# Kernel optimization log

Measured on AMD Instinct MI355X. Metric: run time of the kernel, lower is better.

## Reference

```python
import jax, jax.numpy as jnp
import numpy as np

DIM = 768
HEADS = 16
HEAD_DIM = DIM // HEADS  # 48


def setup_inputs() -> dict:
    key = jax.random.key(0)
    ks = jax.random.split(key, 9)
    s = 1.0 / np.sqrt(DIM)
    inp = {
        "x": jax.random.normal(ks[0], (4, 2048, DIM), dtype=jnp.float32),
        "Wq": jax.random.uniform(ks[1], (DIM, DIM), jnp.float32, -s, s),
        "bq": jax.random.uniform(ks[2], (DIM,), jnp.float32, -s, s),
        "Wk": jax.random.uniform(ks[3], (DIM, DIM), jnp.float32, -s, s),
        "bk": jax.random.uniform(ks[4], (DIM,), jnp.float32, -s, s),
        "Wv": jax.random.uniform(ks[5], (DIM, DIM), jnp.float32, -s, s),
        "bv": jax.random.uniform(ks[6], (DIM,), jnp.float32, -s, s),
        "Wo": jax.random.uniform(ks[7], (DIM, DIM), jnp.float32, -s, s),
        "bo": jax.random.uniform(ks[8], (DIM,), jnp.float32, -s, s),
    }
    return inp


def reference(x, Wq, bq, Wk, bk, Wv, bv, Wo, bo):
    B, S, _ = x.shape
    # torch nn.Linear: y = x @ W.T + b
    q = x @ Wq.T + bq
    k = x @ Wk.T + bk
    v = x @ Wv.T + bv
    # split heads: (B, H, S, Dh)
    q = q.reshape(B, S, HEADS, HEAD_DIM).transpose(0, 2, 1, 3)
    k = k.reshape(B, S, HEADS, HEAD_DIM).transpose(0, 2, 1, 3)
    v = v.reshape(B, S, HEADS, HEAD_DIM).transpose(0, 2, 1, 3)
    score = jnp.einsum("bhqd,bhkd->bhqk", q, k) / jnp.sqrt(jnp.float32(HEAD_DIM))
    attn = jax.nn.softmax(score, axis=-1)
    out = jnp.einsum("bhqk,bhkd->bhqd", attn, v)
    out = out.transpose(0, 2, 1, 3).reshape(B, S, DIM)
    return out @ Wo.T + bo
```

## Files before the change

kernel.cpp:

```cpp
#include <hip/hip_runtime.h>

#define DIM 768
#define SEQ 2048
#define NB 4
#define NH 16
#define DH 48
#define DP 64
#define BHN (NB*NH)
#define MTOK (NB*SEQ)

typedef __attribute__((ext_vector_type(8))) short bf16x8;
typedef __attribute__((ext_vector_type(4))) float f32x4;
typedef __attribute__((ext_vector_type(4))) unsigned int u32x4;

__device__ __forceinline__ unsigned short f32_to_bf16(float f) {
    union { float f; unsigned int u; } v; v.f = f;
    unsigned int r = v.u + 0x7fff + ((v.u >> 16) & 1);
    return (unsigned short)(r >> 16);
}

#if __has_builtin(__builtin_amdgcn_exp2f)
#define EXP2F(x) __builtin_amdgcn_exp2f(x)
#else
#define EXP2F(x) exp2f(x)
#endif

#define GL_LDS16(g, l) __builtin_amdgcn_global_load_lds( \
    (const __attribute__((address_space(1))) void*)(g),  \
    (__attribute__((address_space(3))) void*)(l), 16, 0, 0)

__global__ void cvt_f32_bf16(const float* __restrict__ src, unsigned short* __restrict__ dst, int n) {
    int i = (blockIdx.x * blockDim.x + threadIdx.x) * 4;
    if (i + 3 < n) {
        const float4 v = *(const float4*)(src + i);
        ushort4 o;
        o.x = f32_to_bf16(v.x); o.y = f32_to_bf16(v.y);
        o.z = f32_to_bf16(v.z); o.w = f32_to_bf16(v.w);
        *(ushort4*)(dst + i) = o;
    }
}

__global__ void cvt4_f32_bf16(const float* __restrict__ a, const float* __restrict__ b,
                              const float* __restrict__ c, const float* __restrict__ d,
                              unsigned short* __restrict__ dst, int n_each) {
    const float* srcs[4] = {a, b, c, d};
    const float* src = srcs[blockIdx.y];
    unsigned short* out = dst + blockIdx.y * n_each;
    int i = (blockIdx.x * blockDim.x + threadIdx.x) * 4;
    if (i + 3 < n_each) {
        const float4 v = *(const float4*)(src + i);
        ushort4 o;
        o.x = f32_to_bf16(v.x); o.y = f32_to_bf16(v.y);
        o.z = f32_to_bf16(v.z); o.w = f32_to_bf16(v.w);
        *(ushort4*)(out + i) = o;
    }
}

#define BK 32

__global__ __launch_bounds__(256) void qkv_gemm(
    const unsigned short* __restrict__ xb,
    const unsigned short* __restrict__ wb,
    const float* __restrict__ bq, const float* __restrict__ bk, const float* __restrict__ bv,
    unsigned short* __restrict__ Qb, unsigned short* __restrict__ Kb, unsigned short* __restrict__ Vt)
{
    const int z = blockIdx.z;
    const unsigned short* W = wb + z * (DIM * DIM);
    const float* bias = (z == 0) ? bq : (z == 1) ? bk : bv;
    const int row0 = blockIdx.x * 128;
    const int col0 = blockIdx.y * 128;

    __shared__ __align__(16) short As[128 * BK];
    __shared__ __align__(16) short Bs[128 * BK];

    const int tid = threadIdx.x;
    const int lane = tid & 63;
    const int w = tid >> 6;
    const int wy = w >> 1, wx = w & 1;
    const int l15 = lane & 15, quad = lane >> 4;
    const int lr = lane >> 2;
    const int lco = (lane & 3) * 8;

    f32x4 acc[4][4];
    for (int mi = 0; mi < 4; ++mi) for (int ni = 0; ni < 4; ++ni)
        for (int r = 0; r < 4; ++r) acc[mi][ni][r] = 0.f;

    for (int kt = 0; kt < DIM / BK; ++kt) {
        #pragma unroll
        for (int j = 0; j < 2; ++j) {
            const int c = w * 2 + j;
            GL_LDS16(&xb[(row0 + c * 16 + lr) * DIM + kt * BK + lco], &As[c * 512]);
            GL_LDS16(&W [(col0 + c * 16 + lr) * DIM + kt * BK + lco], &Bs[c * 512]);
        }
        __syncthreads();
        bf16x8 af[4], bfr[4];
        #pragma unroll
        for (int mi = 0; mi < 4; ++mi)
            af[mi] = *(const bf16x8*)&As[(wy * 64 + mi * 16 + l15) * BK + quad * 8];
        #pragma unroll
        for (int ni = 0; ni < 4; ++ni)
            bfr[ni] = *(const bf16x8*)&Bs[(wx * 64 + ni * 16 + l15) * BK + quad * 8];
        #pragma unroll
        for (int mi = 0; mi < 4; ++mi)
            #pragma unroll
            for (int ni = 0; ni < 4; ++ni)
                acc[mi][ni] = __builtin_amdgcn_mfma_f32_16x16x32_bf16(af[mi], bfr[ni], acc[mi][ni], 0, 0, 0);
        __syncthreads();
    }

    const float qscale = 0.14433756729740643f * 1.4426950408889634f;

    if (z == 2) {
        #pragma unroll
        for (int mi = 0; mi < 4; ++mi) {
            #pragma unroll
            for (int ni = 0; ni < 4; ++ni) {
                int col = col0 + wx * 64 + ni * 16 + l15;
                int h = col / DH, d = col - h * DH;
                int row = row0 + wy * 64 + mi * 16 + quad * 4;
                int b = row >> 11, s = row & 2047;
                float bi = bias[col];
                union { ushort4 v; unsigned short e[4]; } pk;
                #pragma unroll
                for (int r = 0; r < 4; ++r)
                    pk.e[r] = f32_to_bf16(acc[mi][ni][r] + bi);
                *(ushort4*)&Vt[((b * NH + h) * DP + d) * SEQ + s] = pk.v;
            }
        }
    } else {
        #pragma unroll
        for (int mi = 0; mi < 4; ++mi) {
            #pragma unroll
            for (int ni = 0; ni < 4; ++ni) {
                #pragma unroll
                for (int r = 0; r < 4; ++r) {
                    int row = row0 + wy * 64 + mi * 16 + quad * 4 + r;
                    int col = col0 + wx * 64 + ni * 16 + l15;
                    float v = acc[mi][ni][r] + bias[col];
                    int b = row >> 11, s = row & 2047;
                    int h = col / DH, d = col - h * DH;
                    int bh = b * NH + h;
                    if (z == 0) Qb[(bh * SEQ + s) * DP + d] = f32_to_bf16(v * qscale);
                    else        Kb[(bh * SEQ + s) * DP + d] = f32_to_bf16(v);
                }
            }
        }
    }
}

__global__ __launch_bounds__(256) void out_gemm(
    const unsigned short* __restrict__ ab,
    const unsigned short* __restrict__ Wo,
    const float* __restrict__ bo,
    float* __restrict__ out)
{
    const int row0 = blockIdx.x * 128;
    const int col0 = blockIdx.y * 128;

    __shared__ __align__(16) short As[128 * BK];
    __shared__ __align__(16) short Bs[128 * BK];

    const int tid = threadIdx.x;
    const int lane = tid & 63;
    const int w = tid >> 6;
    const int wy = w >> 1, wx = w & 1;
    const int l15 = lane & 15, quad = lane >> 4;
    const int lr = lane >> 2;
    const int lco = (lane & 3) * 8;

    f32x4 acc[4][4];
    for (int mi = 0; mi < 4; ++mi) for (int ni = 0; ni < 4; ++ni)
        for (int r = 0; r < 4; ++r) acc[mi][ni][r] = 0.f;

    for (int kt = 0; kt < DIM / BK; ++kt) {
        #pragma unroll
        for (int j = 0; j < 2; ++j) {
            const int c = w * 2 + j;
            GL_LDS16(&ab[(row0 + c * 16 + lr) * DIM + kt * BK + lco], &As[c * 512]);
            GL_LDS16(&Wo[(col0 + c * 16 + lr) * DIM + kt * BK + lco], &Bs[c * 512]);
        }
        __syncthreads();
        bf16x8 af[4], bfr[4];
        #pragma unroll
        for (int mi = 0; mi < 4; ++mi)
            af[mi] = *(const bf16x8*)&As[(wy * 64 + mi * 16 + l15) * BK + quad * 8];
        #pragma unroll
        for (int ni = 0; ni < 4; ++ni)
            bfr[ni] = *(const bf16x8*)&Bs[(wx * 64 + ni * 16 + l15) * BK + quad * 8];
        #pragma unroll
        for (int mi = 0; mi < 4; ++mi)
            #pragma unroll
            for (int ni = 0; ni < 4; ++ni)
                acc[mi][ni] = __builtin_amdgcn_mfma_f32_16x16x32_bf16(af[mi], bfr[ni], acc[mi][ni], 0, 0, 0);
        __syncthreads();
    }

    #pragma unroll
    for (int mi = 0; mi < 4; ++mi)
        #pragma unroll
        for (int ni = 0; ni < 4; ++ni)
            #pragma unroll
            for (int r = 0; r < 4; ++r) {
                int row = row0 + wy * 64 + mi * 16 + quad * 4 + r;
                int col = col0 + wx * 64 + ni * 16 + l15;
                out[row * DIM + col] = acc[mi][ni][r] + bo[col];
            }
}

__device__ __forceinline__ int keyperm(int a) {
    return (a & 32) + ((a & 12) << 1) + ((a & 16) >> 2) + (a & 3);
}

__global__ __launch_bounds__(256, 2) void attn_kernel(
    const unsigned short* __restrict__ Qb,
    const unsigned short* __restrict__ Kb,
    const unsigned short* __restrict__ Vt,
    unsigned short* __restrict__ Ob)
{
    const int bh = blockIdx.x;
    const int tile = blockIdx.y;
    const int tid = threadIdx.x;
    const int w = tid >> 6;
    const int lane = tid & 63;
    const int l15 = lane & 15, quad = lane >> 4;

    const unsigned short* Qh = Qb + bh * SEQ * DP;
    const unsigned short* Kh = Kb + bh * SEQ * DP;
    const unsigned short* Vh = Vt + bh * DP * SEQ;
    const int q0 = tile * 256 + w * 64;

    __shared__ __align__(16) short Ks[64 * 64];
    __shared__ __align__(16) short Vs[48 * 64];

    bf16x8 aq[4][2];
    #pragma unroll
    for (int m = 0; m < 4; ++m)
        #pragma unroll
        for (int ks = 0; ks < 2; ++ks)
            aq[m][ks] = *(const bf16x8*)&Qh[(q0 + m * 16 + l15) * DP + ks * 32 + quad * 8];
    if (quad >= 2) {
        const bf16x8 z8 = {0, 0, 0, 0, 0, 0, 0, 0};
        #pragma unroll
        for (int m = 0; m < 4; ++m) aq[m][1] = z8;
    }

    f32x4 o[4][3];
    #pragma unroll
    for (int m = 0; m < 4; ++m) for (int ni = 0; ni < 3; ++ni)
        for (int r = 0; r < 4; ++r) o[m][ni][r] = 0.f;
    float ls[4][2];
    #pragma unroll
    for (int m = 0; m < 4; ++m) { ls[m][0] = 0.f; ls[m][1] = 0.f; }

    const f32x4 FZ = {0.f, 0.f, 0.f, 0.f};

    const int ra = tid >> 2;
    const int pc = tid & 3;
    const int lcA = ((pc ^ (ra & 7)) * 8);
    const int lcB = (((pc + 4) ^ (ra & 7)) * 8);
    const int kaR = keyperm(ra);
    const int ldsA = ra * 64 + pc * 8;
    const int ldsB = ra * 64 + (pc + 4) * 8;
    const bool vld = (tid < 192);

    bf16x8 kr0, kr1, vr0, vr1;
    kr0 = *(const bf16x8*)&Kh[kaR * DP + lcA];
    kr1 = *(const bf16x8*)&Kh[kaR * DP + lcB];
    if (vld) {
        vr0 = *(const bf16x8*)&Vh[ra * SEQ + lcA];
        vr1 = *(const bf16x8*)&Vh[ra * SEQ + lcB];
    }

    for (int kt = 0; kt < SEQ / 64; ++kt) {
        __syncthreads();
        *(bf16x8*)&Ks[ldsA] = kr0;
        *(bf16x8*)&Ks[ldsB] = kr1;
        if (vld) {
            *(bf16x8*)&Vs[ldsA] = vr0;
            *(bf16x8*)&Vs[ldsB] = vr1;
        }
        if (kt + 1 < SEQ / 64) {
            const int k0n = (kt + 1) * 64;
            kr0 = *(const bf16x8*)&Kh[(k0n + kaR) * DP + lcA];
            kr1 = *(const bf16x8*)&Kh[(k0n + kaR) * DP + lcB];
            if (vld) {
                vr0 = *(const bf16x8*)&Vh[ra * SEQ + k0n + lcA];
                vr1 = *(const bf16x8*)&Vh[ra * SEQ + k0n + lcB];
            }
        }
        __syncthreads();

        bf16x8 ak0[4], ak1[4];
        #pragma unroll
        for (int n = 0; n < 4; ++n) {
            ak0[n] = *(const bf16x8*)&Ks[(n * 16 + l15) * 64 + ((quad ^ (l15 & 7)) * 8)];
            ak1[n] = *(const bf16x8*)&Ks[(n * 16 + l15) * 64 + (((4 + quad) ^ (l15 & 7)) * 8)];
        }
        bf16x8 av[2][3];
        #pragma unroll
        for (int ks = 0; ks < 2; ++ks)
            #pragma unroll
            for (int mt = 0; mt < 3; ++mt)
                av[ks][mt] = *(const bf16x8*)&Vs[(mt * 16 + l15) * 64 + (((ks * 4 + quad) ^ (l15 & 7)) * 8)];

        #pragma unroll
        for (int mp = 0; mp < 2; ++mp) {
            const int m0 = 2 * mp, m1 = 2 * mp + 1;
            f32x4 sc[2][4];
            #pragma unroll
            for (int n = 0; n < 4; ++n) {
                sc[0][n] = __builtin_amdgcn_mfma_f32_16x16x32_bf16(ak0[n], aq[m0][0], FZ, 0, 0, 0);
                sc[1][n] = __builtin_amdgcn_mfma_f32_16x16x32_bf16(ak0[n], aq[m1][0], FZ, 0, 0, 0);
            }
            #pragma unroll
            for (int n = 0; n < 4; ++n) {
                sc[0][n] = __builtin_amdgcn_mfma_f32_16x16x32_bf16(ak1[n], aq[m0][1], sc[0][n], 0, 0, 0);
                sc[1][n] = __builtin_amdgcn_mfma_f32_16x16x32_bf16(ak1[n], aq[m1][1], sc[1][n], 0, 0, 0);
            }
            union { u32x4 u; bf16x8 h; } bp[2][2];
            #pragma unroll
            for (int mi = 0; mi < 2; ++mi) {
                #pragma unroll
                for (int ks = 0; ks < 2; ++ks) {
                    #pragma unroll
                    for (int w2 = 0; w2 < 4; ++w2) {
                        const int j0 = 2 * w2, j1 = 2 * w2 + 1;
                        float p0 = EXP2F(sc[mi][2 * ks + (j0 >> 2)][j0 & 3]);
                        float p1 = EXP2F(sc[mi][2 * ks + (j1 >> 2)][j1 & 3]);
                        ls[2 * mp + mi][w2 & 1] += (p0 + p1);
                        bp[mi][ks].u[w2] = __builtin_amdgcn_perm(__float_as_uint(p1), __float_as_uint(p0), 0x07060302u);
                    }
                }
            }
            #pragma unroll
            for (int ks = 0; ks < 2; ++ks)
                #pragma unroll
                for (int mt = 0; mt < 3; ++mt) {
                    o[m0][mt] = __builtin_amdgcn_mfma_f32_16x16x32_bf16(av[ks][mt], bp[0][ks].h, o[m0][mt], 0, 0, 0);
                    o[m1][mt] = __builtin_amdgcn_mfma_f32_16x16x32_bf16(av[ks][mt], bp[1][ks].h, o[m1][mt], 0, 0, 0);
                }
        }
    }

    const int b = bh >> 4, h = bh & 15;
    #pragma unroll
    for (int m = 0; m < 4; ++m) {
        float lsum = ls[m][0] + ls[m][1];
        lsum += __shfl_xor(lsum, 16);
        lsum += __shfl_xor(lsum, 32);
        float inv = 1.f / lsum;
        #pragma unroll
        for (int mt = 0; mt < 3; ++mt)
            #pragma unroll
            for (int r = 0; r < 4; ++r) {
                int token = b * SEQ + q0 + m * 16 + l15;
                int d = mt * 16 + quad * 4 + r;
                Ob[token * DIM + h * DH + d] = f32_to_bf16(o[m][mt][r] * inv);
            }
    }
}

extern "C" void kernel_launch(void* const* d_in, const int* in_sizes, int n_in,
                              void* d_out, int out_size, void* d_ws, size_t ws_size,
                              hipStream_t stream) {
    const float* x  = (const float*)d_in[0];
    const float* Wq = (const float*)d_in[1]; const float* bq = (const float*)d_in[2];
    const float* Wk = (const float*)d_in[3]; const float* bk = (const float*)d_in[4];
    const float* Wv = (const float*)d_in[5]; const float* bv = (const float*)d_in[6];
    const float* Wo = (const float*)d_in[7]; const float* bo = (const float*)d_in[8];

    unsigned char* ws = (unsigned char*)d_ws;
    unsigned short* xb = (unsigned short*)(ws);
    unsigned short* wb = (unsigned short*)(ws + 12582912);
    unsigned short* Qb = (unsigned short*)(ws + 17301504);
    unsigned short* Kb = (unsigned short*)(ws + 34078720);
    unsigned short* Vt = (unsigned short*)(ws + 50855936);
    unsigned short* Ob = (unsigned short*)(ws + 67633152);

    cvt_f32_bf16<<<6144, 256, 0, stream>>>(x, xb, MTOK * DIM);
    cvt4_f32_bf16<<<dim3(576, 4), 256, 0, stream>>>(Wq, Wk, Wv, Wo, wb, DIM * DIM);

    qkv_gemm<<<dim3(MTOK / 128, DIM / 128, 3), 256, 0, stream>>>(xb, wb, bq, bk, bv, Qb, Kb, Vt);
    attn_kernel<<<dim3(BHN, SEQ / 256), 256, 0, stream>>>(Qb, Kb, Vt, Ob);
    out_gemm<<<dim3(MTOK / 128, DIM / 128), 256, 0, stream>>>(Ob, wb + 3 * DIM * DIM, bo, (float*)d_out);
}
```

Before: 218.9 us.

## Halve attention query tile per block, raise occupancy, add MFMA priority hints

The attention kernel now processes 128 queries per block (32 per wave) instead of 256, doubling the grid and raising launch bounds to 4 blocks per CU to increase occupancy and parallelism. MFMA sections are wrapped in s_setprio to favor matrix issue across waves, and output stores are packed into ushort4 vector writes. The trade-off is that each K/V tile loaded into LDS is reused by half as many queries, doubling K/V global and LDS traffic.

```diff
diff --git a/kernel.cpp b/kernel.cpp
--- a/kernel.cpp
+++ b/kernel.cpp
@@ -211,7 +211,7 @@
     return (a & 32) + ((a & 12) << 1) + ((a & 16) >> 2) + (a & 3);
 }
 
-__global__ __launch_bounds__(256, 2) void attn_kernel(
+__global__ __launch_bounds__(256, 4) void attn_kernel(
     const unsigned short* __restrict__ Qb,
     const unsigned short* __restrict__ Kb,
     const unsigned short* __restrict__ Vt,
@@ -227,30 +227,30 @@
     const unsigned short* Qh = Qb + bh * SEQ * DP;
     const unsigned short* Kh = Kb + bh * SEQ * DP;
     const unsigned short* Vh = Vt + bh * DP * SEQ;
-    const int q0 = tile * 256 + w * 64;
+    const int q0 = tile * 128 + w * 32;
 
     __shared__ __align__(16) short Ks[64 * 64];
     __shared__ __align__(16) short Vs[48 * 64];
 
-    bf16x8 aq[4][2];
-    #pragma unroll
-    for (int m = 0; m < 4; ++m)
+    bf16x8 aq[2][2];
+    #pragma unroll
+    for (int m = 0; m < 2; ++m)
         #pragma unroll
         for (int ks = 0; ks < 2; ++ks)
             aq[m][ks] = *(const bf16x8*)&Qh[(q0 + m * 16 + l15) * DP + ks * 32 + quad * 8];
     if (quad >= 2) {
         const bf16x8 z8 = {0, 0, 0, 0, 0, 0, 0, 0};
         #pragma unroll
-        for (int m = 0; m < 4; ++m) aq[m][1] = z8;
-    }
-
-    f32x4 o[4][3];
-    #pragma unroll
-    for (int m = 0; m < 4; ++m) for (int ni = 0; ni < 3; ++ni)
+        for (int m = 0; m < 2; ++m) aq[m][1] = z8;
+    }
+
+    f32x4 o[2][3];
+    #pragma unroll
+    for (int m = 0; m < 2; ++m) for (int ni = 0; ni < 3; ++ni)
         for (int r = 0; r < 4; ++r) o[m][ni][r] = 0.f;
-    float ls[4][2];
-    #pragma unroll
-    for (int m = 0; m < 4; ++m) { ls[m][0] = 0.f; ls[m][1] = 0.f; }
+    float ls[2][2];
+    #pragma unroll
+    for (int m = 0; m < 2; ++m) { ls[m][0] = 0.f; ls[m][1] = 0.f; }
 
     const f32x4 FZ = {0.f, 0.f, 0.f, 0.f};
 
@@ -303,60 +303,61 @@
             for (int mt = 0; mt < 3; ++mt)
                 av[ks][mt] = *(const bf16x8*)&Vs[(mt * 16 + l15) * 64 + (((ks * 4 + quad) ^ (l15 & 7)) * 8)];
 
-        #pragma unroll
-        for (int mp = 0; mp < 2; ++mp) {
-            const int m0 = 2 * mp, m1 = 2 * mp + 1;
-            f32x4 sc[2][4];
-            #pragma unroll
-            for (int n = 0; n < 4; ++n) {
-                sc[0][n] = __builtin_amdgcn_mfma_f32_16x16x32_bf16(ak0[n], aq[m0][0], FZ, 0, 0, 0);
-                sc[1][n] = __builtin_amdgcn_mfma_f32_16x16x32_bf16(ak0[n], aq[m1][0], FZ, 0, 0, 0);
-            }
-            #pragma unroll
-            for (int n = 0; n < 4; ++n) {
-                sc[0][n] = __builtin_amdgcn_mfma_f32_16x16x32_bf16(ak1[n], aq[m0][1], sc[0][n], 0, 0, 0);
-                sc[1][n] = __builtin_amdgcn_mfma_f32_16x16x32_bf16(ak1[n], aq[m1][1], sc[1][n], 0, 0, 0);
-            }
-            union { u32x4 u; bf16x8 h; } bp[2][2];
-            #pragma unroll
-            for (int mi = 0; mi < 2; ++mi) {
+        f32x4 sc[2][4];
+        __builtin_amdgcn_s_setprio(1);
+        #pragma unroll
+        for (int n = 0; n < 4; ++n) {
+            sc[0][n] = __builtin_amdgcn_mfma_f32_16x16x32_bf16(ak0[n], aq[0][0], FZ, 0, 0, 0);
+            sc[1][n] = __builtin_amdgcn_mfma_f32_16x16x32_bf16(ak0[n], aq[1][0], FZ, 0, 0, 0);
+        }
+        #pragma unroll
+        for (int n = 0; n < 4; ++n) {
+            sc[0][n] = __builtin_amdgcn_mfma_f32_16x16x32_bf16(ak1[n], aq[0][1], sc[0][n], 0, 0, 0);
+            sc[1][n] = __builtin_amdgcn_mfma_f32_16x16x32_bf16(ak1[n], aq[1][1], sc[1][n], 0, 0, 0);
+        }
+        __builtin_amdgcn_s_setprio(0);
+        union { u32x4 u; bf16x8 h; } bp[2][2];
+        #pragma unroll
+        for (int mi = 0; mi < 2; ++mi) {
+            #pragma unroll
+            for (int ks = 0; ks < 2; ++ks) {
                 #pragma unroll
-                for (int ks = 0; ks < 2; ++ks) {
-                    #pragma unroll
-                    for (int w2 = 0; w2 < 4; ++w2) {
-                        const int j0 = 2 * w2, j1 = 2 * w2 + 1;
-                        float p0 = EXP2F(sc[mi][2 * ks + (j0 >> 2)][j0 & 3]);
-                        float p1 = EXP2F(sc[mi][2 * ks + (j1 >> 2)][j1 & 3]);
-                        ls[2 * mp + mi][w2 & 1] += (p0 + p1);
-                        bp[mi][ks].u[w2] = __builtin_amdgcn_perm(__float_as_uint(p1), __float_as_uint(p0), 0x07060302u);
-                    }
+                for (int w2 = 0; w2 < 4; ++w2) {
+                    const int j0 = 2 * w2, j1 = 2 * w2 + 1;
+                    float p0 = EXP2F(sc[mi][2 * ks + (j0 >> 2)][j0 & 3]);
+                    float p1 = EXP2F(sc[mi][2 * ks + (j1 >> 2)][j1 & 3]);
+                    ls[mi][w2 & 1] += (p0 + p1);
+                    bp[mi][ks].u[w2] = __builtin_amdgcn_perm(__float_as_uint(p1), __float_as_uint(p0), 0x07060302u);
                 }
             }
-            #pragma unroll
-            for (int ks = 0; ks < 2; ++ks)
-                #pragma unroll
-                for (int mt = 0; mt < 3; ++mt) {
-                    o[m0][mt] = __builtin_amdgcn_mfma_f32_16x16x32_bf16(av[ks][mt], bp[0][ks].h, o[m0][mt], 0, 0, 0);
-                    o[m1][mt] = __builtin_amdgcn_mfma_f32_16x16x32_bf16(av[ks][mt], bp[1][ks].h, o[m1][mt], 0, 0, 0);
-                }
-        }
+        }
+        __builtin_amdgcn_s_setprio(1);
+        #pragma unroll
+        for (int ks = 0; ks < 2; ++ks)
+            #pragma unroll
+            for (int mt = 0; mt < 3; ++mt) {
+                o[0][mt] = __builtin_amdgcn_mfma_f32_16x16x32_bf16(av[ks][mt], bp[0][ks].h, o[0][mt], 0, 0, 0);
+                o[1][mt] = __builtin_amdgcn_mfma_f32_16x16x32_bf16(av[ks][mt], bp[1][ks].h, o[1][mt], 0, 0, 0);
+            }
+        __builtin_amdgcn_s_setprio(0);
     }
 
     const int b = bh >> 4, h = bh & 15;
     #pragma unroll
-    for (int m = 0; m < 4; ++m) {
+    for (int m = 0; m < 2; ++m) {
         float lsum = ls[m][0] + ls[m][1];
         lsum += __shfl_xor(lsum, 16);
         lsum += __shfl_xor(lsum, 32);
         float inv = 1.f / lsum;
-        #pragma unroll
-        for (int mt = 0; mt < 3; ++mt)
-            #pragma unroll
-            for (int r = 0; r < 4; ++r) {
-                int token = b * SEQ + q0 + m * 16 + l15;
-                int d = mt * 16 + quad * 4 + r;
-                Ob[token * DIM + h * DH + d] = f32_to_bf16(o[m][mt][r] * inv);
-            }
+        int token = b * SEQ + q0 + m * 16 + l15;
+        #pragma unroll
+        for (int mt = 0; mt < 3; ++mt) {
+            union { ushort4 v; unsigned short e[4]; } pk;
+            #pragma unroll
+            for (int r = 0; r < 4; ++r)
+                pk.e[r] = f32_to_bf16(o[m][mt][r] * inv);
+            *(ushort4*)&Ob[token * DIM + h * DH + mt * 16 + quad * 4] = pk.v;
+        }
     }
 }
 
@@ -381,6 +382,6 @@
     cvt4_f32_bf16<<<dim3(576, 4), 256, 0, stream>>>(Wq, Wk, Wv, Wo, wb, DIM * DIM);
 
     qkv_gemm<<<dim3(MTOK / 128, DIM / 128, 3), 256, 0, stream>>>(xb, wb, bq, bk, bv, Qb, Kb, Vt);
-    attn_kernel<<<dim3(BHN, SEQ / 256), 256, 0, stream>>>(Qb, Kb, Vt, Ob);
+    attn_kernel<<<dim3(BHN, SEQ / 128), 256, 0, stream>>>(Qb, Kb, Vt, Ob);
     out_gemm<<<dim3(MTOK / 128, DIM / 128), 256, 0, stream>>>(Ob, wb + 3 * DIM * DIM, bo, (float*)d_out);
 }
```

Result: slower. 304.6 us (+39.1%).

## Split attention keys across wave pairs with direct-to-LDS loads and LDS merge

Applied to the files above, without the earlier changes.

Each block now handles 128 queries: two waves cover the query halves and two wave-groups each process half of the key range. The partial outputs and row sums are merged through shared memory at the end, and the grid is doubled. K/V tiles are loaded with direct global-to-LDS copies (GL_LDS16) instead of register staging. The change also adds s_setprio around the MFMA sections and vectorized bf16 output stores. This raises the block count and parallelism, at the cost of reloading K/V per block and an extra reduction step. The occupancy hint of two blocks per CU is dropped from the launch bounds.

```diff
diff --git a/kernel.cpp b/kernel.cpp
--- a/kernel.cpp
+++ b/kernel.cpp
@@ -211,7 +211,7 @@
     return (a & 32) + ((a & 12) << 1) + ((a & 16) >> 2) + (a & 3);
 }
 
-__global__ __launch_bounds__(256, 2) void attn_kernel(
+__global__ __launch_bounds__(256) void attn_kernel(
     const unsigned short* __restrict__ Qb,
     const unsigned short* __restrict__ Kb,
     const unsigned short* __restrict__ Vt,
@@ -221,16 +221,19 @@
     const int tile = blockIdx.y;
     const int tid = threadIdx.x;
     const int w = tid >> 6;
+    const int qg = w & 1;
+    const int kh = w >> 1;
     const int lane = tid & 63;
     const int l15 = lane & 15, quad = lane >> 4;
 
     const unsigned short* Qh = Qb + bh * SEQ * DP;
     const unsigned short* Kh = Kb + bh * SEQ * DP;
     const unsigned short* Vh = Vt + bh * DP * SEQ;
-    const int q0 = tile * 256 + w * 64;
-
-    __shared__ __align__(16) short Ks[64 * 64];
-    __shared__ __align__(16) short Vs[48 * 64];
+    const int q0 = tile * 128 + qg * 64;
+
+    __shared__ __align__(16) short SMEM[2 * 64 * 64 + 2 * 48 * 64];
+    short* KsH = SMEM + kh * (64 * 64);
+    short* VsH = SMEM + 2 * 64 * 64 + kh * (48 * 64);
 
     bf16x8 aq[4][2];
     #pragma unroll
@@ -254,59 +257,49 @@
 
     const f32x4 FZ = {0.f, 0.f, 0.f, 0.f};
 
-    const int ra = tid >> 2;
-    const int pc = tid & 3;
-    const int lcA = ((pc ^ (ra & 7)) * 8);
-    const int lcB = (((pc + 4) ^ (ra & 7)) * 8);
-    const int kaR = keyperm(ra);
-    const int ldsA = ra * 64 + pc * 8;
-    const int ldsB = ra * 64 + (pc + 4) * 8;
-    const bool vld = (tid < 192);
-
-    bf16x8 kr0, kr1, vr0, vr1;
-    kr0 = *(const bf16x8*)&Kh[kaR * DP + lcA];
-    kr1 = *(const bf16x8*)&Kh[kaR * DP + lcB];
-    if (vld) {
-        vr0 = *(const bf16x8*)&Vh[ra * SEQ + lcA];
-        vr1 = *(const bf16x8*)&Vh[ra * SEQ + lcB];
-    }
-
-    for (int kt = 0; kt < SEQ / 64; ++kt) {
-        __syncthreads();
-        *(bf16x8*)&Ks[ldsA] = kr0;
-        *(bf16x8*)&Ks[ldsB] = kr1;
-        if (vld) {
-            *(bf16x8*)&Vs[ldsA] = vr0;
-            *(bf16x8*)&Vs[ldsB] = vr1;
-        }
-        if (kt + 1 < SEQ / 64) {
-            const int k0n = (kt + 1) * 64;
-            kr0 = *(const bf16x8*)&Kh[(k0n + kaR) * DP + lcA];
-            kr1 = *(const bf16x8*)&Kh[(k0n + kaR) * DP + lcB];
-            if (vld) {
-                vr0 = *(const bf16x8*)&Vh[ra * SEQ + k0n + lcA];
-                vr1 = *(const bf16x8*)&Vh[ra * SEQ + k0n + lcB];
-            }
-        }
+    const int lr3 = lane >> 3, pcc = lane & 7;
+    const int swz8 = (pcc ^ lr3) * 8;
+    int kso[4], vso[3];
+    #pragma unroll
+    for (int j = 0; j < 4; ++j) {
+        const int ra = (qg * 4 + j) * 8 + lr3;
+        kso[j] = keyperm(ra) * DP + swz8;
+    }
+    #pragma unroll
+    for (int j = 0; j < 3; ++j) {
+        const int ra = (qg * 3 + j) * 8 + lr3;
+        vso[j] = ra * SEQ + swz8;
+    }
+
+    for (int kt = 0; kt < SEQ / 128; ++kt) {
+        const int k0 = (kh * (SEQ / 128) + kt) * 64;
+        __syncthreads();
+        #pragma unroll
+        for (int j = 0; j < 4; ++j)
+            GL_LDS16(&Kh[k0 * DP + kso[j]], &KsH[(qg * 4 + j) * 512]);
+        #pragma unroll
+        for (int j = 0; j < 3; ++j)
+            GL_LDS16(&Vh[k0 + vso[j]], &VsH[(qg * 3 + j) * 512]);
         __syncthreads();
 
         bf16x8 ak0[4], ak1[4];
         #pragma unroll
         for (int n = 0; n < 4; ++n) {
-            ak0[n] = *(const bf16x8*)&Ks[(n * 16 + l15) * 64 + ((quad ^ (l15 & 7)) * 8)];
-            ak1[n] = *(const bf16x8*)&Ks[(n * 16 + l15) * 64 + (((4 + quad) ^ (l15 & 7)) * 8)];
+            ak0[n] = *(const bf16x8*)&KsH[(n * 16 + l15) * 64 + ((quad ^ (l15 & 7)) * 8)];
+            ak1[n] = *(const bf16x8*)&KsH[(n * 16 + l15) * 64 + (((4 + quad) ^ (l15 & 7)) * 8)];
         }
         bf16x8 av[2][3];
         #pragma unroll
         for (int ks = 0; ks < 2; ++ks)
             #pragma unroll
             for (int mt = 0; mt < 3; ++mt)
-                av[ks][mt] = *(const bf16x8*)&Vs[(mt * 16 + l15) * 64 + (((ks * 4 + quad) ^ (l15 & 7)) * 8)];
+                av[ks][mt] = *(const bf16x8*)&VsH[(mt * 16 + l15) * 64 + (((ks * 4 + quad) ^ (l15 & 7)) * 8)];
 
         #pragma unroll
         for (int mp = 0; mp < 2; ++mp) {
             const int m0 = 2 * mp, m1 = 2 * mp + 1;
             f32x4 sc[2][4];
+            __builtin_amdgcn_s_setprio(1);
             #pragma unroll
             for (int n = 0; n < 4; ++n) {
                 sc[0][n] = __builtin_amdgcn_mfma_f32_16x16x32_bf16(ak0[n], aq[m0][0], FZ, 0, 0, 0);
@@ -317,6 +310,7 @@
                 sc[0][n] = __builtin_amdgcn_mfma_f32_16x16x32_bf16(ak1[n], aq[m0][1], sc[0][n], 0, 0, 0);
                 sc[1][n] = __builtin_amdgcn_mfma_f32_16x16x32_bf16(ak1[n], aq[m1][1], sc[1][n], 0, 0, 0);
             }
+            __builtin_amdgcn_s_setprio(0);
             union { u32x4 u; bf16x8 h; } bp[2][2];
             #pragma unroll
             for (int mi = 0; mi < 2; ++mi) {
@@ -332,6 +326,7 @@
                     }
                 }
             }
+            __builtin_amdgcn_s_setprio(1);
             #pragma unroll
             for (int ks = 0; ks < 2; ++ks)
                 #pragma unroll
@@ -339,24 +334,51 @@
                     o[m0][mt] = __builtin_amdgcn_mfma_f32_16x16x32_bf16(av[ks][mt], bp[0][ks].h, o[m0][mt], 0, 0, 0);
                     o[m1][mt] = __builtin_amdgcn_mfma_f32_16x16x32_bf16(av[ks][mt], bp[1][ks].h, o[m1][mt], 0, 0, 0);
                 }
-        }
-    }
-
-    const int b = bh >> 4, h = bh & 15;
-    #pragma unroll
-    for (int m = 0; m < 4; ++m) {
-        float lsum = ls[m][0] + ls[m][1];
-        lsum += __shfl_xor(lsum, 16);
-        lsum += __shfl_xor(lsum, 32);
-        float inv = 1.f / lsum;
-        #pragma unroll
-        for (int mt = 0; mt < 3; ++mt)
-            #pragma unroll
-            for (int r = 0; r < 4; ++r) {
-                int token = b * SEQ + q0 + m * 16 + l15;
-                int d = mt * 16 + quad * 4 + r;
-                Ob[token * DIM + h * DH + d] = f32_to_bf16(o[m][mt][r] * inv);
-            }
+            __builtin_amdgcn_s_setprio(0);
+        }
+    }
+
+    __syncthreads();
+    float* sh = (float*)SMEM;
+    if (kh == 1) {
+        float* dst = sh + qg * 3584 + lane;
+        #pragma unroll
+        for (int m = 0; m < 4; ++m) {
+            #pragma unroll
+            for (int mt = 0; mt < 3; ++mt)
+                #pragma unroll
+                for (int r = 0; r < 4; ++r)
+                    dst[((m * 3 + mt) * 4 + r) * 64] = o[m][mt][r];
+            dst[(48 + 2 * m) * 64] = ls[m][0];
+            dst[(49 + 2 * m) * 64] = ls[m][1];
+        }
+    }
+    __syncthreads();
+    if (kh == 0) {
+        const float* src = sh + qg * 3584 + lane;
+        const int b = bh >> 4, h = bh & 15;
+        #pragma unroll
+        for (int m = 0; m < 4; ++m) {
+            #pragma unroll
+            for (int mt = 0; mt < 3; ++mt)
+                #pragma unroll
+                for (int r = 0; r < 4; ++r)
+                    o[m][mt][r] += src[((m * 3 + mt) * 4 + r) * 64];
+            float lsum = (ls[m][0] + src[(48 + 2 * m) * 64])
+                       + (ls[m][1] + src[(49 + 2 * m) * 64]);
+            lsum += __shfl_xor(lsum, 16);
+            lsum += __shfl_xor(lsum, 32);
+            float inv = 1.f / lsum;
+            int token = b * SEQ + q0 + m * 16 + l15;
+            #pragma unroll
+            for (int mt = 0; mt < 3; ++mt) {
+                union { ushort4 v; unsigned short e[4]; } pk;
+                #pragma unroll
+                for (int r = 0; r < 4; ++r)
+                    pk.e[r] = f32_to_bf16(o[m][mt][r] * inv);
+                *(ushort4*)&Ob[token * DIM + h * DH + mt * 16 + quad * 4] = pk.v;
+            }
+        }
     }
 }
 
@@ -381,6 +403,6 @@
     cvt4_f32_bf16<<<dim3(576, 4), 256, 0, stream>>>(Wq, Wk, Wv, Wo, wb, DIM * DIM);
 
     qkv_gemm<<<dim3(MTOK / 128, DIM / 128, 3), 256, 0, stream>>>(xb, wb, bq, bk, bv, Qb, Kb, Vt);
-    attn_kernel<<<dim3(BHN, SEQ / 256), 256, 0, stream>>>(Qb, Kb, Vt, Ob);
+    attn_kernel<<<dim3(BHN, SEQ / 128), 256, 0, stream>>>(Qb, Kb, Vt, Ob);
     out_gemm<<<dim3(MTOK / 128, DIM / 128), 256, 0, stream>>>(Ob, wb + 3 * DIM * DIM, bo, (float*)d_out);
 }
```

Result: slower. 278.8 us (+27.4%).
